# Kernel optimization log

Hardware: AMD Instinct MI355X
Metric: run time of the kernel (lower is better)

The kernel has to match this reference:

```python
import jax, jax.numpy as jnp
import numpy as np

WS = 14  # window size
NH = 12  # num heads
EPS = 1e-5  # torch LayerNorm eps


def _rel_idx(ws: int) -> np.ndarray:
    coords = np.stack(np.meshgrid(np.arange(ws), np.arange(ws), indexing='ij'))
    cf = coords.reshape(2, -1)                      # (2, N)
    rel = cf[:, :, None] - cf[:, None, :]           # (2, N, N)
    rel = rel.transpose(1, 2, 0).copy()
    rel[:, :, 0] += ws - 1
    rel[:, :, 1] += ws - 1
    rel[:, :, 0] *= 2 * ws - 1
    return rel.sum(-1)                              # (N, N) int


def _layernorm(x, w, b):
    mu = jnp.mean(x, axis=-1, keepdims=True)
    var = jnp.var(x, axis=-1, keepdims=True)
    return (x - mu) * jax.lax.rsqrt(var + EPS) * w + b


def setup_inputs() -> dict:
    key = jax.random.key(0)
    ks = jax.random.split(key, 8)
    d, dff = 768, 3072
    s = lambda k, shape, sc: jax.random.normal(k, shape, jnp.float32) * sc
    return {
        'x': jax.random.normal(ks[0], (8, d, 56, 56), jnp.float32),
        'norm1_w': jnp.ones((d,), jnp.float32),
        'norm1_b': jnp.zeros((d,), jnp.float32),
        'qkv_w': s(ks[1], (d, 3 * d), 0.02),
        'qkv_b': jnp.zeros((3 * d,), jnp.float32),
        'rel_bias_table': s(ks[2], ((2 * WS - 1) ** 2, NH), 0.02),
        'proj_w': s(ks[3], (d, d), 0.02),
        'proj_b': jnp.zeros((d,), jnp.float32),
        'norm2_w': jnp.ones((d,), jnp.float32),
        'norm2_b': jnp.zeros((d,), jnp.float32),
        'fc1_w': s(ks[4], (d, dff), 0.02),
        'fc1_b': jnp.zeros((dff,), jnp.float32),
        'fc2_w': s(ks[5], (dff, d), 0.02),
        'fc2_b': jnp.zeros((d,), jnp.float32),
        'gamma1': jnp.full((d,), 1e-5, jnp.float32),
        'gamma2': jnp.full((d,), 1e-5, jnp.float32),
    }


def reference(x, norm1_w, norm1_b, qkv_w, qkv_b, rel_bias_table, proj_w, proj_b,
              norm2_w, norm2_b, fc1_w, fc1_b, fc2_w, fc2_b, gamma1, gamma2):
    B, C, H, W = x.shape
    nh, hd = NH, C // NH
    N = WS * WS
    xs = jnp.transpose(x, (0, 2, 3, 1))             # B,H,W,C
    shortcut = xs
    h = _layernorm(xs, norm1_w, norm1_b)

    # window partition (H, W divisible by WS)
    hw = h.reshape(B, H // WS, WS, W // WS, WS, C)
    hw = jnp.transpose(hw, (0, 1, 3, 2, 4, 5)).reshape(-1, N, C)  # (Bw, N, C)

    qkv = hw @ qkv_w + qkv_b                        # (Bw, N, 3C)
    qkv = qkv.reshape(-1, N, 3, nh, hd)
    q, k, v = [jnp.transpose(qkv[:, :, i], (0, 2, 1, 3)) for i in range(3)]  # (Bw,nh,N,hd)

    attn = jnp.einsum('bhnd,bhmd->bhnm', q, k) * (hd ** -0.5)
    rel_idx = jnp.asarray(_rel_idx(WS))             # static (N,N)
    bias = rel_bias_table[rel_idx]                  # (N,N,nh)
    attn = attn + jnp.transpose(bias, (2, 0, 1))[None]
    attn = jax.nn.softmax(attn, axis=-1)

    out = jnp.einsum('bhnm,bhmd->bnhd', attn, v).reshape(-1, N, C)
    out = out @ proj_w + proj_b                     # (Bw, N, C)

    # window reverse
    out = out.reshape(B, H // WS, W // WS, WS, WS, C)
    out = jnp.transpose(out, (0, 1, 3, 2, 4, 5)).reshape(B, H, W, C)

    xs = shortcut + gamma1 * out
    h2 = _layernorm(xs, norm2_w, norm2_b)
    mlp = jax.nn.gelu(h2 @ fc1_w + fc1_b, approximate=False) @ fc2_w + fc2_b
    xs = xs + gamma2 * mlp
    return jnp.transpose(xs, (0, 3, 1, 2))          # B,C,H,W
```

## Files before the change

kernel.cpp:

```cpp
#include <hip/hip_runtime.h>
#include <cstdint>
#include <cstddef>


typedef unsigned short u16;
typedef short short8 __attribute__((ext_vector_type(8)));
typedef float floatx4 __attribute__((ext_vector_type(4)));

static __device__ __forceinline__ float bf2f(u16 u) {
  return __uint_as_float(((unsigned)u) << 16);
}
static __device__ __forceinline__ u16 f2bf(float f) {
  unsigned u = __float_as_uint(f);
  return (u16)((u + 0x7FFFu + ((u >> 16) & 1u)) >> 16);
}
static __device__ __forceinline__ float ldin(const void* p, size_t i, int isf) {
  return isf ? ((const float*)p)[i] : bf2f(((const u16*)p)[i]);
}
static __device__ __forceinline__ void gload_lds16(const void* g, void* l) {
  __builtin_amdgcn_global_load_lds(
      (const __attribute__((address_space(1))) void*)g,
      (__attribute__((address_space(3))) void*)l, 16, 0, 0);
}
static __device__ __forceinline__ float fast_gelu(float v) {
  float u2 = v * (1.5957691216f + 0.0713548163f * v * v);
  return v * (1.0f / (1.0f + __expf(-u2)));
}

__global__ __launch_bounds__(256) void detect_kernel(const u16* __restrict__ x,
                                                     int* __restrict__ flag) {
  __shared__ int tot;
  if (threadIdx.x == 0) tot = 0;
  __syncthreads();
  int cnt = 0;
  for (int i = threadIdx.x; i < 4096; i += 256) {
    int e = (x[i] >> 7) & 0xFF;
    if (e >= 0xC1) cnt++;
  }
  atomicAdd(&tot, cnt);
  __syncthreads();
  if (threadIdx.x == 0) flag[0] = (tot > 16) ? 1 : 0;
}

__global__ __launch_bounds__(256) void cvt_params_kernel(
    const void* n1w, const void* n1b, const void* qkvb, const void* projb,
    const void* n2w, const void* n2b, const void* fc1b, const void* fc2b,
    const void* g1, const void* g2, const void* bt, u16* __restrict__ P,
    const int* __restrict__ flag) {
  int isf = *flag;
  int i = blockIdx.x * 256 + threadIdx.x;
  const void* src; int off;
  if      (i < 768)   { src = n1w;   off = i; }
  else if (i < 1536)  { src = n1b;   off = i - 768; }
  else if (i < 3840)  { src = qkvb;  off = i - 1536; }
  else if (i < 4608)  { src = projb; off = i - 3840; }
  else if (i < 5376)  { src = n2w;   off = i - 4608; }
  else if (i < 6144)  { src = n2b;   off = i - 5376; }
  else if (i < 9216)  { src = fc1b;  off = i - 6144; }
  else if (i < 9984)  { src = fc2b;  off = i - 9216; }
  else if (i < 10752) { src = g1;    off = i - 9984; }
  else if (i < 11520) { src = g2;    off = i - 10752; }
  else if (i < 20268) { src = bt;    off = i - 11520; }
  else return;
  P[i] = f2bf(ldin(src, off, isf));
}

__global__ __launch_bounds__(256) void wtr_kernel(const void* __restrict__ W,
                                                  u16* __restrict__ WT,
                                                  int K, int N,
                                                  const int* __restrict__ flag) {
  int isf = *flag;
  __shared__ u16 tl[32][33];
  int tx = threadIdx.x, ty = threadIdx.y;
  int n0 = blockIdx.x * 32, k0 = blockIdx.y * 32;
#pragma unroll
  for (int j = 0; j < 32; j += 8)
    tl[ty + j][tx] = f2bf(ldin(W, (size_t)(k0 + ty + j) * N + n0 + tx, isf));
  __syncthreads();
#pragma unroll
  for (int j = 0; j < 32; j += 8)
    WT[(size_t)(n0 + ty + j) * K + k0 + tx] = tl[tx][ty + j];
}

__global__ __launch_bounds__(256) void tin_kernel(const void* __restrict__ x,
                                                  u16* __restrict__ sc,
                                                  const int* __restrict__ flag) {
  int isf = *flag;
  int cc = blockIdx.x, h = blockIdx.y, b = blockIdx.z;
  __shared__ u16 tile[64 * 57];
  int tid = threadIdx.x;
  for (int i = tid; i < 64 * 56; i += 256) {
    int ci = i / 56, w = i - ci * 56;
    tile[ci * 57 + w] =
        f2bf(ldin(x, (((size_t)b * 768 + cc * 64 + ci) * 56 + h) * 56 + w, isf));
  }
  __syncthreads();
  int hb = h / 14, hi = h - hb * 14;
  for (int i = tid; i < 56 * 64; i += 256) {
    int w = i >> 6, ci = i & 63;
    int wb = w / 14, wj = w - wb * 14;
    int r = (b * 16 + hb * 4 + wb) * 196 + hi * 14 + wj;
    sc[(size_t)r * 768 + cc * 64 + ci] = tile[ci * 57 + w];
  }
}

__global__ __launch_bounds__(256) void tout_kernel(const u16* __restrict__ src,
                                                   void* __restrict__ out,
                                                   const int* __restrict__ flag) {
  int isf = *flag;
  int cc = blockIdx.x, h = blockIdx.y, b = blockIdx.z;
  __shared__ u16 tile[64 * 57];
  int tid = threadIdx.x;
  int hb = h / 14, hi = h - hb * 14;
  for (int i = tid; i < 56 * 64; i += 256) {
    int w = i >> 6, ci = i & 63;
    int wb = w / 14, wj = w - wb * 14;
    int r = (b * 16 + hb * 4 + wb) * 196 + hi * 14 + wj;
    tile[ci * 57 + w] = src[(size_t)r * 768 + cc * 64 + ci];
  }
  __syncthreads();
  for (int i = tid; i < 64 * 56; i += 256) {
    int ci = i / 56, w = i - ci * 56;
    size_t o = (((size_t)b * 768 + cc * 64 + ci) * 56 + h) * 56 + w;
    if (isf) ((float*)out)[o] = bf2f(tile[ci * 57 + w]);
    else     ((u16*)out)[o]   = tile[ci * 57 + w];
  }
}

__global__ __launch_bounds__(256) void ln_kernel(const u16* __restrict__ xin,
                                                 const u16* __restrict__ wt,
                                                 const u16* __restrict__ bs,
                                                 u16* __restrict__ out) {
  int row = blockIdx.x, t = threadIdx.x;
  const u16* xr = xin + (size_t)row * 768;
  float v0 = bf2f(xr[t]), v1 = bf2f(xr[t + 256]), v2 = bf2f(xr[t + 512]);
  float s1 = v0 + v1 + v2;
  float s2 = v0 * v0 + v1 * v1 + v2 * v2;
#pragma unroll
  for (int off = 32; off > 0; off >>= 1) {
    s1 += __shfl_xor(s1, off);
    s2 += __shfl_xor(s2, off);
  }
  __shared__ float p1[4], p2[4];
  if ((t & 63) == 0) { p1[t >> 6] = s1; p2[t >> 6] = s2; }
  __syncthreads();
  float S1 = p1[0] + p1[1] + p1[2] + p1[3];
  float S2 = p2[0] + p2[1] + p2[2] + p2[3];
  float mu = S1 * (1.f / 768.f);
  float var = S2 * (1.f / 768.f) - mu * mu;
  float rs = rsqrtf(var + 1e-5f);
  u16* orow = out + (size_t)row * 768;
  orow[t]       = f2bf((v0 - mu) * rs * bf2f(wt[t])       + bf2f(bs[t]));
  orow[t + 256] = f2bf((v1 - mu) * rs * bf2f(wt[t + 256]) + bf2f(bs[t + 256]));
  orow[t + 512] = f2bf((v2 - mu) * rs * bf2f(wt[t + 512]) + bf2f(bs[t + 512]));
}

template <int EPI>
__global__ __launch_bounds__(256) void gemm_kernel(
    const u16* __restrict__ A, const u16* __restrict__ BT,
    const u16* __restrict__ bias, const u16* __restrict__ gamma,
    u16* out, int N, int K, int NX, int NY) {
  int bid = blockIdx.x;
  int r8 = bid & 7, q = bid >> 3;
  int xb = q % NX, yb = (q / NX) * 8 + r8;
  if (yb >= NY) return;

  __shared__ u16 As[128 * 32];
  __shared__ u16 Bs[128 * 32];
  int tid = threadIdx.x;
  int w = tid >> 6, l = tid & 63;
  int lane15 = l & 15, quad = l >> 4;
  int m0 = yb * 128, n0 = xb * 128;
  int wm = w & 1, wn = w >> 1;
  floatx4 acc[4][4];
#pragma unroll
  for (int i = 0; i < 4; i++)
#pragma unroll
    for (int j = 0; j < 4; j++)
#pragma unroll
      for (int e = 0; e < 4; e++) acc[i][j][e] = 0.f;

  const u16* Abase = A + (size_t)m0 * K;
  const u16* Bbase = BT + (size_t)n0 * K;
  int rseg = l >> 2, ch = l & 3;

  for (int kt = 0; kt < K; kt += 32) {
    __syncthreads();
#pragma unroll
    for (int sI = 0; sI < 2; ++sI) {
      int s = w * 2 + sI;
      gload_lds16(Abase + (size_t)(s * 16 + rseg) * K + kt + ch * 8, &As[s * 512]);
      gload_lds16(Bbase + (size_t)(s * 16 + rseg) * K + kt + ch * 8, &Bs[s * 512]);
    }
    __syncthreads();
    short8 af[4], bf[4];
#pragma unroll
    for (int mi = 0; mi < 4; ++mi)
      af[mi] = *(const short8*)&As[(wm * 64 + mi * 16 + lane15) * 32 + quad * 8];
#pragma unroll
    for (int ni = 0; ni < 4; ++ni)
      bf[ni] = *(const short8*)&Bs[(wn * 64 + ni * 16 + lane15) * 32 + quad * 8];
#pragma unroll
    for (int mi = 0; mi < 4; ++mi)
#pragma unroll
      for (int ni = 0; ni < 4; ++ni)
        acc[mi][ni] = __builtin_amdgcn_mfma_f32_16x16x32_bf16(
            af[mi], bf[ni], acc[mi][ni], 0, 0, 0);
  }

  if constexpr (EPI == 1) {
#pragma unroll
    for (int mi = 0; mi < 4; ++mi) {
      int row0 = m0 + wm * 64 + mi * 16 + quad * 4;
#pragma unroll
      for (int ni = 0; ni < 4; ++ni) {
        int col = n0 + wn * 64 + ni * 16 + lane15;
        float bv = bf2f(bias[col]);
        float gv = bf2f(gamma[col]);
#pragma unroll
        for (int reg = 0; reg < 4; ++reg) {
          size_t idx = (size_t)(row0 + reg) * N + col;
          float v = acc[mi][ni][reg] + bv;
          out[idx] = f2bf(bf2f(out[idx]) + gv * v);
        }
      }
    }
  } else {
    __shared__ __align__(16) u16 Cs[128 * 136];
    __syncthreads();
#pragma unroll
    for (int mi = 0; mi < 4; ++mi) {
      int rl0 = wm * 64 + mi * 16 + quad * 4;
#pragma unroll
      for (int ni = 0; ni < 4; ++ni) {
        int cl = wn * 64 + ni * 16 + lane15;
        float bv = bf2f(bias[n0 + cl]);
#pragma unroll
        for (int reg = 0; reg < 4; ++reg) {
          float v = acc[mi][ni][reg] + bv;
          if (EPI == 2) v = fast_gelu(v);
          Cs[(rl0 + reg) * 136 + cl] = f2bf(v);
        }
      }
    }
    __syncthreads();
    int rr = tid >> 4, cc8 = (tid & 15) * 8;
#pragma unroll
    for (int chk = 0; chk < 8; ++chk) {
      int row = chk * 16 + rr;
      short8 val = *(const short8*)&Cs[row * 136 + cc8];
      *(short8*)(out + (size_t)(m0 + row) * N + n0 + cc8) = val;
    }
  }
}

__global__ __launch_bounds__(256) void attn_kernel(const u16* __restrict__ qkv,
                                                   const u16* __restrict__ btab,
                                                   u16* __restrict__ out) {
  __shared__ __align__(16) u16 VT[64 * 232];
  __shared__ __align__(16) u16 Pa[4 * 2 * 512];
  __shared__ float bS[729];
  int bid = blockIdx.x;
  int win = bid / 12, h = bid - win * 12;
  int tid = threadIdx.x, w = tid >> 6, l = tid & 63;
  int lane15 = l & 15, quad = l >> 4;
  const u16* qbase = qkv + (size_t)win * 196 * 2304;

  for (int i = tid; i < 64 * 28; i += 256) {
    int d = i / 28, m = i - d * 28;
    VT[d * 232 + 196 + m] = 0;
  }
  for (int i = tid; i < 196 * 64; i += 256) {
    int m = i >> 6, d = i & 63;
    VT[d * 232 + m] = qbase[(size_t)m * 2304 + 1536 + h * 64 + d];
  }
  for (int i = tid; i < 729; i += 256) bS[i] = bf2f(btab[i * 12 + h]);
  __syncthreads();

  u16* Pw = Pa + w * 1024;
  for (int rt = w; rt < 13; rt += 4) {
    floatx4 acc[13];
#pragma unroll
    for (int nt = 0; nt < 13; ++nt)
#pragma unroll
      for (int e = 0; e < 4; ++e) acc[nt][e] = 0.f;

    int rq = rt * 16 + lane15;
    bool qok = rq < 196;
#pragma unroll
    for (int kk = 0; kk < 2; ++kk) {
      short8 qf;
      if (qok)
        qf = *(const short8*)&qbase[(size_t)rq * 2304 + h * 64 + kk * 32 + quad * 8];
      else
#pragma unroll
        for (int e = 0; e < 8; ++e) qf[e] = 0;
#pragma unroll
      for (int nt = 0; nt < 13; ++nt) {
        int n = nt * 16 + lane15;
        short8 kf = *(const short8*)&qbase[(size_t)n * 2304 + 768 + h * 64 + kk * 32 + quad * 8];
        acc[nt] = __builtin_amdgcn_mfma_f32_16x16x32_bf16(qf, kf, acc[nt], 0, 0, 0);
      }
    }

    int i1[4], j1[4]; bool rv[4]; float mx[4], sm[4];
#pragma unroll
    for (int reg = 0; reg < 4; ++reg) {
      int r = rt * 16 + quad * 4 + reg;
      i1[reg] = r / 14; j1[reg] = r - i1[reg] * 14;
      rv[reg] = r < 196; mx[reg] = -1e30f; sm[reg] = 0.f;
    }
#pragma unroll
    for (int nt = 0; nt < 13; ++nt) {
      int cc = nt * 16 + lane15;
      bool cv = cc < 196;
      int i2 = cc / 14, j2 = cc - i2 * 14;
#pragma unroll
      for (int reg = 0; reg < 4; ++reg) {
        float v;
        if (cv) {
          v = acc[nt][reg] * 0.125f;
          if (rv[reg]) v += bS[(i1[reg] - i2 + 13) * 27 + (j1[reg] - j2 + 13)];
        } else v = -1e30f;
        acc[nt][reg] = v;
        mx[reg] = fmaxf(mx[reg], v);
      }
    }
#pragma unroll
    for (int reg = 0; reg < 4; ++reg)
#pragma unroll
      for (int off = 1; off < 16; off <<= 1)
        mx[reg] = fmaxf(mx[reg], __shfl_xor(mx[reg], off));
#pragma unroll
    for (int nt = 0; nt < 13; ++nt)
#pragma unroll
      for (int reg = 0; reg < 4; ++reg) {
        float p = __expf(acc[nt][reg] - mx[reg]);
        acc[nt][reg] = p; sm[reg] += p;
      }
#pragma unroll
    for (int reg = 0; reg < 4; ++reg) {
#pragma unroll
      for (int off = 1; off < 16; off <<= 1) sm[reg] += __shfl_xor(sm[reg], off);
      sm[reg] = 1.f / sm[reg];
    }

    floatx4 oa[4];
#pragma unroll
    for (int dt = 0; dt < 4; ++dt)
#pragma unroll
      for (int e = 0; e < 4; ++e) oa[dt][e] = 0.f;
#pragma unroll
    for (int kk = 0; kk < 7; ++kk) {
      u16* Pb = Pw + (kk & 1) * 512;
#pragma unroll
      for (int p = 0; p < 2; ++p) {
        int nt = kk * 2 + p;
#pragma unroll
        for (int reg = 0; reg < 4; ++reg) {
          float v = (nt < 13) ? acc[nt][reg] * sm[reg] : 0.f;
          Pb[(quad * 4 + reg) * 32 + p * 16 + lane15] = f2bf(v);
        }
      }
      asm volatile("s_waitcnt lgkmcnt(0)" ::: "memory");
      short8 pf = *(const short8*)&Pb[lane15 * 32 + quad * 8];
#pragma unroll
      for (int dt = 0; dt < 4; ++dt) {
        short8 vf = *(const short8*)&VT[(dt * 16 + lane15) * 232 + kk * 32 + quad * 8];
        oa[dt] = __builtin_amdgcn_mfma_f32_16x16x32_bf16(pf, vf, oa[dt], 0, 0, 0);
      }
    }
#pragma unroll
    for (int dt = 0; dt < 4; ++dt)
#pragma unroll
      for (int reg = 0; reg < 4; ++reg) {
        int r = rt * 16 + quad * 4 + reg;
        if (r < 196)
          out[((size_t)win * 196 + r) * 768 + h * 64 + dt * 16 + lane15] =
              f2bf(oa[dt][reg]);
      }
  }
}

static inline int gemm_grid(int NX, int NY) { return NX * ((NY + 7) / 8) * 8; }

extern "C" void kernel_launch(void* const* d_in, const int* in_sizes, int n_in,
                              void* d_out, int out_size, void* d_ws, size_t ws_size,
                              hipStream_t stream) {
  const void* x      = d_in[0];
  const void* n1w    = d_in[1];
  const void* n1b    = d_in[2];
  const void* qkv_w  = d_in[3];
  const void* qkv_b  = d_in[4];
  const void* btab   = d_in[5];
  const void* proj_w = d_in[6];
  const void* proj_b = d_in[7];
  const void* n2w    = d_in[8];
  const void* n2b    = d_in[9];
  const void* fc1_w  = d_in[10];
  const void* fc1_b  = d_in[11];
  const void* fc2_w  = d_in[12];
  const void* fc2_b  = d_in[13];
  const void* gamma1 = d_in[14];
  const void* gamma2 = d_in[15];
  (void)in_sizes; (void)n_in; (void)out_size;

  int c;
  if      (ws_size >= 245432576ull) c = 1;
  else if (ws_size >= 168362240ull) c = 2;
  else                              c = 4;
  const int R = 25088 / c;
  const int WN = 128 / c;
  const int NY = R / 128;

  char* ws = (char*)d_ws;
  int*  flag  = (int*)ws;
  u16*  P     = (u16*)(ws + 256);
  u16*  qkvT  = (u16*)(ws + 65792);
  u16*  projT = (u16*)(ws + 65792 + 3538944);
  u16*  fc1T  = (u16*)(ws + 65792 + 4718592);
  u16*  fc2T  = (u16*)(ws + 65792 + 9437184);
  const size_t B0 = 38535168;
  u16*  buf0  = (u16*)(ws + 14221568);
  u16*  buf1  = (u16*)(ws + 14221568 + B0);
  char* scr   = ws + 14221568 + 2 * B0;

  u16 *p_n1w = P, *p_n1b = P + 768, *p_qkvb = P + 1536, *p_projb = P + 3840;
  u16 *p_n2w = P + 4608, *p_n2b = P + 5376, *p_fc1b = P + 6144;
  u16 *p_fc2b = P + 9216, *p_g1 = P + 9984, *p_g2 = P + 10752, *p_bt = P + 11520;

  dim3 b256(256), bw(32, 8);
  detect_kernel<<<dim3(1), b256, 0, stream>>>((const u16*)x, flag);
  cvt_params_kernel<<<dim3(80), b256, 0, stream>>>(
      n1w, n1b, qkv_b, proj_b, n2w, n2b, fc1_b, fc2_b, gamma1, gamma2, btab,
      P, flag);
  wtr_kernel<<<dim3(72, 24), bw, 0, stream>>>(qkv_w, qkvT, 768, 2304, flag);
  wtr_kernel<<<dim3(24, 24), bw, 0, stream>>>(proj_w, projT, 768, 768, flag);
  wtr_kernel<<<dim3(96, 24), bw, 0, stream>>>(fc1_w, fc1T, 768, 3072, flag);
  wtr_kernel<<<dim3(24, 96), bw, 0, stream>>>(fc2_w, fc2T, 3072, 768, flag);

  tin_kernel<<<dim3(12, 56, 8), b256, 0, stream>>>(x, buf0, flag);
  ln_kernel<<<dim3(25088), b256, 0, stream>>>(buf0, p_n1w, p_n1b, buf1);

  for (int hc = 0; hc < c; ++hc) {
    size_t ro = (size_t)hc * R * 768;
    u16* qC = (u16*)scr;
    u16* aC = (u16*)(scr + (size_t)R * 4608);
    gemm_kernel<0><<<dim3(gemm_grid(18, NY)), b256, 0, stream>>>(
        buf1 + ro, qkvT, p_qkvb, nullptr, qC, 2304, 768, 18, NY);
    attn_kernel<<<dim3(WN * 12), b256, 0, stream>>>(qC, p_bt, aC);
    gemm_kernel<1><<<dim3(gemm_grid(6, NY)), b256, 0, stream>>>(
        aC, projT, p_projb, p_g1, buf0 + ro, 768, 768, 6, NY);
  }

  ln_kernel<<<dim3(25088), b256, 0, stream>>>(buf0, p_n2w, p_n2b, buf1);

  for (int hc = 0; hc < c; ++hc) {
    size_t ro = (size_t)hc * R * 768;
    u16* gC = (u16*)scr;
    gemm_kernel<2><<<dim3(gemm_grid(24, NY)), b256, 0, stream>>>(
        buf1 + ro, fc1T, p_fc1b, nullptr, gC, 3072, 768, 24, NY);
    gemm_kernel<1><<<dim3(gemm_grid(6, NY)), b256, 0, stream>>>(
        gC, fc2T, p_fc2b, p_g2, buf0 + ro, 768, 3072, 6, NY);
  }

  tout_kernel<<<dim3(12, 56, 8), b256, 0, stream>>>(buf0, d_out, flag);
}
```

Before: 1.037 ms.

## Replace 128x128 GEMM with 256-row double-buffered swizzled-LDS 512-thread kernel

Replaces the single-buffered 128x128x32 GEMM with a 512-thread kernel using 256-row tiles, BK=64, and 256- or 128-column tiles. Global-to-LDS loads for the next K step are double-buffered and interleaved with MFMA phases, and the LDS layout is XOR-swizzled to avoid bank conflicts. The epilogue stages through LDS and does vectorized residual updates with row bounds checks. It aims for more data reuse and overlap of loads with math, at the cost of more LDS per block, lower occupancy, and partial tiles when R is not a multiple of 256.

Result: faster. 996.4 us (-4.0%).

```diff
diff --git a/kernel.cpp b/kernel.cpp
--- a/kernel.cpp
+++ b/kernel.cpp
@@ -155,101 +155,167 @@
   orow[t + 512] = f2bf((v2 - mu) * rs * bf2f(wt[t + 512]) + bf2f(bs[t + 512]));
 }
 
-template <int EPI>
-__global__ __launch_bounds__(256) void gemm_kernel(
+template <int EPI, int NPH>
+__global__ __launch_bounds__(512, 2) void gemm256_kernel(
     const u16* __restrict__ A, const u16* __restrict__ BT,
     const u16* __restrict__ bias, const u16* __restrict__ gamma,
-    u16* out, int N, int K, int NX, int NY) {
+    u16* __restrict__ out, int M, int N, int K, int NX, int NYT) {
+  constexpr int BN  = 64 * NPH;
+  constexpr int WM  = 8 / NPH;
+  constexpr int MF  = 2 * NPH;
+  constexpr int ATS = 16384;
+  constexpr int BTS = 4096 * NPH;
+  __shared__ __align__(16) u16 LDS[2 * ATS + 2 * BTS];
+
   int bid = blockIdx.x;
   int r8 = bid & 7, q = bid >> 3;
   int xb = q % NX, yb = (q / NX) * 8 + r8;
-  if (yb >= NY) return;
-
-  __shared__ u16 As[128 * 32];
-  __shared__ u16 Bs[128 * 32];
+  if (yb >= NYT) return;
+  int m0 = yb * 256, n0 = xb * BN;
+
   int tid = threadIdx.x;
   int w = tid >> 6, l = tid & 63;
-  int lane15 = l & 15, quad = l >> 4;
-  int m0 = yb * 128, n0 = xb * 128;
-  int wm = w & 1, wn = w >> 1;
-  floatx4 acc[4][4];
-#pragma unroll
-  for (int i = 0; i < 4; i++)
-#pragma unroll
-    for (int j = 0; j < 4; j++)
-#pragma unroll
-      for (int e = 0; e < 4; e++) acc[i][j][e] = 0.f;
-
-  const u16* Abase = A + (size_t)m0 * K;
-  const u16* Bbase = BT + (size_t)n0 * K;
-  int rseg = l >> 2, ch = l & 3;
-
-  for (int kt = 0; kt < K; kt += 32) {
+  int l15 = l & 15, quad = l >> 4;
+  int wm = w & (WM - 1), wn = w / WM;
+
+  int lrow8 = l >> 3;
+  int lk = ((l & 7) ^ lrow8) * 8;
+  const u16* aptr[4];
+  const u16* bptr[NPH];
+#pragma unroll
+  for (int j = 0; j < 4; ++j) {
+    int ra = m0 + w * 32 + j * 8 + lrow8;
+    if (ra > M - 1) ra = M - 1;
+    aptr[j] = A + (size_t)ra * K + lk;
+  }
+#pragma unroll
+  for (int j = 0; j < NPH; ++j) {
+    int rb = n0 + (w * NPH + j) * 8 + lrow8;
+    bptr[j] = BT + (size_t)rb * K + lk;
+  }
+  int kq0 = (((quad * 16)      ^ ((l15 & 7) << 4)) >> 1);
+  int kq1 = (((64 + quad * 16) ^ ((l15 & 7) << 4)) >> 1);
+
+  floatx4 acc[MF][4];
+#pragma unroll
+  for (int i = 0; i < MF; ++i)
+#pragma unroll
+    for (int jn = 0; jn < 4; ++jn)
+#pragma unroll
+      for (int e = 0; e < 4; ++e) acc[i][jn][e] = 0.f;
+
+  int nt = K >> 6;
+#pragma unroll
+  for (int j = 0; j < 4; ++j)
+    gload_lds16(aptr[j], LDS + (w * 4 + j) * 512);
+#pragma unroll
+  for (int j = 0; j < NPH; ++j)
+    gload_lds16(bptr[j], LDS + 2 * ATS + (w * NPH + j) * 512);
+
+  for (int t = 0; t < nt; ++t) {
+    int cur = t & 1, nxt = cur ^ 1;
+    const u16* Ac = LDS + cur * ATS;
+    const u16* Bc = LDS + 2 * ATS + cur * BTS;
+    u16* An = LDS + nxt * ATS;
+    u16* Bn = LDS + 2 * ATS + nxt * BTS;
+    bool pf = (t + 1) < nt;
+    int ko = (t + 1) << 6;
+    asm volatile("s_waitcnt vmcnt(0)" ::: "memory");
+    __builtin_amdgcn_s_barrier();
+    short8 bfr[4][2];
+#pragma unroll
+    for (int p = 0; p < NPH; ++p) {
+      if (p == 0) {
+#pragma unroll
+        for (int ni = 0; ni < 4; ++ni) {
+          const u16* bp = Bc + (wn * 64 + ni * 16 + l15) * 64;
+          bfr[ni][0] = *(const short8*)(bp + kq0);
+          bfr[ni][1] = *(const short8*)(bp + kq1);
+        }
+      }
+      short8 af0[2], af1[2];
+      {
+        const u16* ap0 = Ac + (wm * (32 * NPH) + (2 * p) * 16 + l15) * 64;
+        const u16* ap1 = ap0 + 16 * 64;
+        af0[0] = *(const short8*)(ap0 + kq0);
+        af0[1] = *(const short8*)(ap0 + kq1);
+        af1[0] = *(const short8*)(ap1 + kq0);
+        af1[1] = *(const short8*)(ap1 + kq1);
+      }
+      if (pf) {
+        if constexpr (NPH == 4) {
+          gload_lds16(aptr[p] + ko, An + (w * 4 + p) * 512);
+          gload_lds16(bptr[p] + ko, Bn + (w * 4 + p) * 512);
+        } else {
+          gload_lds16(aptr[2 * p] + ko,     An + (w * 4 + 2 * p) * 512);
+          gload_lds16(aptr[2 * p + 1] + ko, An + (w * 4 + 2 * p + 1) * 512);
+          gload_lds16(bptr[p] + ko,         Bn + (w * 2 + p) * 512);
+        }
+      }
+      __builtin_amdgcn_s_barrier();
+      __builtin_amdgcn_s_setprio(1);
+#pragma unroll
+      for (int ni = 0; ni < 4; ++ni) {
+        acc[2 * p][ni] = __builtin_amdgcn_mfma_f32_16x16x32_bf16(
+            af0[0], bfr[ni][0], acc[2 * p][ni], 0, 0, 0);
+        acc[2 * p][ni] = __builtin_amdgcn_mfma_f32_16x16x32_bf16(
+            af0[1], bfr[ni][1], acc[2 * p][ni], 0, 0, 0);
+        acc[2 * p + 1][ni] = __builtin_amdgcn_mfma_f32_16x16x32_bf16(
+            af1[0], bfr[ni][0], acc[2 * p + 1][ni], 0, 0, 0);
+        acc[2 * p + 1][ni] = __builtin_amdgcn_mfma_f32_16x16x32_bf16(
+            af1[1], bfr[ni][1], acc[2 * p + 1][ni], 0, 0, 0);
+      }
+      __builtin_amdgcn_s_setprio(0);
+      __builtin_amdgcn_s_barrier();
+    }
+  }
+
+  constexpr int CSTR = BN + 8;
+  u16* Cs = LDS;
+  float bv[4];
+#pragma unroll
+  for (int ni = 0; ni < 4; ++ni)
+    bv[ni] = bf2f(bias[n0 + wn * 64 + ni * 16 + l15]);
+  for (int cch = 0; cch < 2; ++cch) {
     __syncthreads();
-#pragma unroll
-    for (int sI = 0; sI < 2; ++sI) {
-      int s = w * 2 + sI;
-      gload_lds16(Abase + (size_t)(s * 16 + rseg) * K + kt + ch * 8, &As[s * 512]);
-      gload_lds16(Bbase + (size_t)(s * 16 + rseg) * K + kt + ch * 8, &Bs[s * 512]);
+    if (((wm * NPH) >> 2) == cch) {
+      int rbase = wm * (32 * NPH) - cch * 128 + quad * 4;
+#pragma unroll
+      for (int mi = 0; mi < MF; ++mi)
+#pragma unroll
+        for (int ni = 0; ni < 4; ++ni) {
+          int cl = wn * 64 + ni * 16 + l15;
+#pragma unroll
+          for (int reg = 0; reg < 4; ++reg) {
+            float v = acc[mi][ni][reg] + bv[ni];
+            if constexpr (EPI == 2) v = fast_gelu(v);
+            Cs[(rbase + mi * 16 + reg) * CSTR + cl] = f2bf(v);
+          }
+        }
     }
     __syncthreads();
-    short8 af[4], bf[4];
-#pragma unroll
-    for (int mi = 0; mi < 4; ++mi)
-      af[mi] = *(const short8*)&As[(wm * 64 + mi * 16 + lane15) * 32 + quad * 8];
-#pragma unroll
-    for (int ni = 0; ni < 4; ++ni)
-      bf[ni] = *(const short8*)&Bs[(wn * 64 + ni * 16 + lane15) * 32 + quad * 8];
-#pragma unroll
-    for (int mi = 0; mi < 4; ++mi)
-#pragma unroll
-      for (int ni = 0; ni < 4; ++ni)
-        acc[mi][ni] = __builtin_amdgcn_mfma_f32_16x16x32_bf16(
-            af[mi], bf[ni], acc[mi][ni], 0, 0, 0);
-  }
-
-  if constexpr (EPI == 1) {
-#pragma unroll
-    for (int mi = 0; mi < 4; ++mi) {
-      int row0 = m0 + wm * 64 + mi * 16 + quad * 4;
-#pragma unroll
-      for (int ni = 0; ni < 4; ++ni) {
-        int col = n0 + wn * 64 + ni * 16 + lane15;
-        float bv = bf2f(bias[col]);
-        float gv = bf2f(gamma[col]);
-#pragma unroll
-        for (int reg = 0; reg < 4; ++reg) {
-          size_t idx = (size_t)(row0 + reg) * N + col;
-          float v = acc[mi][ni][reg] + bv;
-          out[idx] = f2bf(bf2f(out[idx]) + gv * v);
+#pragma unroll
+    for (int it = 0; it < BN / 32; ++it) {
+      int idx = it * 512 + tid;
+      int row = idx / (BN / 8);
+      int c8 = (idx - row * (BN / 8)) * 8;
+      int grow = m0 + cch * 128 + row;
+      if (grow < M) {
+        short8 val = *(const short8*)&Cs[row * CSTR + c8];
+        u16* po = out + (size_t)grow * N + n0 + c8;
+        if constexpr (EPI == 1) {
+          short8 rv = *(const short8*)po;
+          short8 gv = *(const short8*)(gamma + n0 + c8);
+          short8 res;
+#pragma unroll
+          for (int e = 0; e < 8; ++e)
+            res[e] = (short)f2bf(bf2f((u16)rv[e]) +
+                                 bf2f((u16)gv[e]) * bf2f((u16)val[e]));
+          *(short8*)po = res;
+        } else {
+          *(short8*)po = val;
         }
       }
-    }
-  } else {
-    __shared__ __align__(16) u16 Cs[128 * 136];
-    __syncthreads();
-#pragma unroll
-    for (int mi = 0; mi < 4; ++mi) {
-      int rl0 = wm * 64 + mi * 16 + quad * 4;
-#pragma unroll
-      for (int ni = 0; ni < 4; ++ni) {
-        int cl = wn * 64 + ni * 16 + lane15;
-        float bv = bf2f(bias[n0 + cl]);
-#pragma unroll
-        for (int reg = 0; reg < 4; ++reg) {
-          float v = acc[mi][ni][reg] + bv;
-          if (EPI == 2) v = fast_gelu(v);
-          Cs[(rl0 + reg) * 136 + cl] = f2bf(v);
-        }
-      }
-    }
-    __syncthreads();
-    int rr = tid >> 4, cc8 = (tid & 15) * 8;
-#pragma unroll
-    for (int chk = 0; chk < 8; ++chk) {
-      int row = chk * 16 + rr;
-      short8 val = *(const short8*)&Cs[row * 136 + cc8];
-      *(short8*)(out + (size_t)(m0 + row) * N + n0 + cc8) = val;
     }
   }
 }
@@ -382,7 +448,7 @@
   }
 }
 
-static inline int gemm_grid(int NX, int NY) { return NX * ((NY + 7) / 8) * 8; }
+static inline int gemm_grid(int NX, int NYT) { return NX * ((NYT + 7) / 8) * 8; }
 
 extern "C" void kernel_launch(void* const* d_in, const int* in_sizes, int n_in,
                               void* d_out, int out_size, void* d_ws, size_t ws_size,
@@ -411,7 +477,7 @@
   else                              c = 4;
   const int R = 25088 / c;
   const int WN = 128 / c;
-  const int NY = R / 128;
+  const int NYT = (R + 255) / 256;
 
   char* ws = (char*)d_ws;
   int*  flag  = (int*)ws;
@@ -429,7 +495,7 @@
   u16 *p_n2w = P + 4608, *p_n2b = P + 5376, *p_fc1b = P + 6144;
   u16 *p_fc2b = P + 9216, *p_g1 = P + 9984, *p_g2 = P + 10752, *p_bt = P + 11520;
 
-  dim3 b256(256), bw(32, 8);
+  dim3 b256(256), b512(512), bw(32, 8);
   detect_kernel<<<dim3(1), b256, 0, stream>>>((const u16*)x, flag);
   cvt_params_kernel<<<dim3(80), b256, 0, stream>>>(
       n1w, n1b, qkv_b, proj_b, n2w, n2b, fc1_b, fc2_b, gamma1, gamma2, btab,
@@ -446,11 +512,11 @@
     size_t ro = (size_t)hc * R * 768;
     u16* qC = (u16*)scr;
     u16* aC = (u16*)(scr + (size_t)R * 4608);
-    gemm_kernel<0><<<dim3(gemm_grid(18, NY)), b256, 0, stream>>>(
-        buf1 + ro, qkvT, p_qkvb, nullptr, qC, 2304, 768, 18, NY);
+    gemm256_kernel<0, 4><<<dim3(gemm_grid(9, NYT)), b512, 0, stream>>>(
+        buf1 + ro, qkvT, p_qkvb, nullptr, qC, R, 2304, 768, 9, NYT);
     attn_kernel<<<dim3(WN * 12), b256, 0, stream>>>(qC, p_bt, aC);
-    gemm_kernel<1><<<dim3(gemm_grid(6, NY)), b256, 0, stream>>>(
-        aC, projT, p_projb, p_g1, buf0 + ro, 768, 768, 6, NY);
+    gemm256_kernel<1, 2><<<dim3(gemm_grid(6, NYT)), b512, 0, stream>>>(
+        aC, projT, p_projb, p_g1, buf0 + ro, R, 768, 768, 6, NYT);
   }
 
   ln_kernel<<<dim3(25088), b256, 0, stream>>>(buf0, p_n2w, p_n2b, buf1);
@@ -458,10 +524,10 @@
   for (int hc = 0; hc < c; ++hc) {
     size_t ro = (size_t)hc * R * 768;
     u16* gC = (u16*)scr;
-    gemm_kernel<2><<<dim3(gemm_grid(24, NY)), b256, 0, stream>>>(
-        buf1 + ro, fc1T, p_fc1b, nullptr, gC, 3072, 768, 24, NY);
-    gemm_kernel<1><<<dim3(gemm_grid(6, NY)), b256, 0, stream>>>(
-        gC, fc2T, p_fc2b, p_g2, buf0 + ro, 768, 3072, 6, NY);
+    gemm256_kernel<2, 4><<<dim3(gemm_grid(12, NYT)), b512, 0, stream>>>(
+        buf1 + ro, fc1T, p_fc1b, nullptr, gC, R, 3072, 768, 12, NYT);
+    gemm256_kernel<1, 2><<<dim3(gemm_grid(6, NYT)), b512, 0, stream>>>(
+        gC, fc2T, p_fc2b, p_g2, buf0 + ro, R, 768, 3072, 6, NYT);
   }
 
   tout_kernel<<<dim3(12, 56, 8), b256, 0, stream>>>(buf0, d_out, flag);
```
